# Performance work log

Measured on AMD Instinct MI355X. Metric: run time of the kernel, lower is better.

Reference implementation:

```python
import jax, jax.numpy as jnp
import numpy as np

N_NODES = 100000
N_EDGES = 3200000
N_FEATS = 512
HIDDEN = 16
N_CLASSES = 40


def gcn_conv(x, edge_index, W, b):
    """PyG-style GCNConv: linear -> symmetric-normalized scatter-add -> bias."""
    n = x.shape[0]
    src, dst = edge_index[0], edge_index[1]
    # add self-loops
    loop = jnp.arange(n, dtype=src.dtype)
    src = jnp.concatenate([src, loop])
    dst = jnp.concatenate([dst, loop])
    # symmetric normalization deg^{-1/2}[src] * deg^{-1/2}[dst]
    deg = jax.ops.segment_sum(jnp.ones_like(src, dtype=x.dtype), dst, num_segments=n)
    dinv = jnp.where(deg > 0, jax.lax.rsqrt(jnp.maximum(deg, 1.0)), 0.0)
    norm = dinv[src] * dinv[dst]  # [E+N]
    h = x @ W                     # [N, out]
    msg = h[src] * norm[:, None]  # gather + scale, [E+N, out]
    out = jax.ops.segment_sum(msg, dst, num_segments=n)  # scatter-add at targets
    return out + b


def setup_inputs() -> dict:
    key = jax.random.key(0)
    k1, k2, k3, k4 = jax.random.split(key, 4)
    x = jax.random.normal(k1, (N_NODES, N_FEATS), dtype=jnp.float32)
    edge_index = jax.random.randint(k2, (2, N_EDGES), 0, N_NODES, dtype=jnp.int64)
    # Glorot-ish scaled weights
    W1 = jax.random.normal(k3, (N_FEATS, HIDDEN), dtype=jnp.float32) * (1.0 / np.sqrt(N_FEATS))
    b1 = jnp.zeros((HIDDEN,), dtype=jnp.float32)
    W2 = jax.random.normal(k4, (HIDDEN, N_CLASSES), dtype=jnp.float32) * (1.0 / np.sqrt(HIDDEN))
    b2 = jnp.zeros((N_CLASSES,), dtype=jnp.float32)
    return {"x": x, "edge_index": edge_index, "W1": W1, "b1": b1, "W2": W2, "b2": b2}


def reference(x, edge_index, W1, b1, W2, b2):
    h = gcn_conv(x, edge_index, W1, b1)
    h = jax.nn.relu(h)
    # dropout is identity in eval mode
    h = gcn_conv(h, edge_index, W2, b2)
    return jax.nn.log_softmax(h, axis=1)
```

## Files before the change

kernel.cpp:

```cpp
#include <hip/hip_runtime.h>
#include <hip/hip_bf16.h>

#define NN 100000
#define NE 3200000
#define NF 512
#define NH 16
#define NC 40
#define NB 782
#define CAP 5120
#define NBLK 512
#define CHUNK 6250

typedef __attribute__((ext_vector_type(4))) float f32x4;
typedef __attribute__((ext_vector_type(8))) short bf16x8;

static __device__ __forceinline__ unsigned short f2b(float f) {
    unsigned int u = __float_as_uint(f);
    u += 0x7FFFu + ((u >> 16) & 1u);
    return (unsigned short)(u >> 16);
}
static __device__ __forceinline__ float b2f(unsigned short u) {
    return __uint_as_float(((unsigned int)u) << 16);
}


__global__ void __launch_bounds__(256) k_mshist(const int* __restrict__ ei,
                                                int* __restrict__ histG) {
    __shared__ int h[NB];
    for (int i = threadIdx.x; i < NB; i += 256) h[i] = 0;
    __syncthreads();
    int b = blockIdx.x;
    int e0 = b * CHUNK, e1 = min(NE, e0 + CHUNK);
    for (int e = e0 + threadIdx.x; e < e1; e += 256)
        atomicAdd(&h[((unsigned)ei[NE + e]) >> 7], 1);
    __syncthreads();
    for (int i = threadIdx.x; i < NB; i += 256)
        histG[b * NB + i] = h[i];
}


__global__ void __launch_bounds__(512) k_colscan(const int* __restrict__ histG,
                                                 int* __restrict__ ofsG,
                                                 int* __restrict__ bcnt) {
    __shared__ int sh[NBLK];
    int k = blockIdx.x;
    int t = threadIdx.x;
    int v = histG[t * NB + k];
    sh[t] = v;
    __syncthreads();
    for (int off = 1; off < NBLK; off <<= 1) {
        int add = (t >= off) ? sh[t - off] : 0;
        __syncthreads();
        sh[t] += add;
        __syncthreads();
    }
    ofsG[k * NBLK + t] = sh[t] - v;
    if (t == NBLK - 1) bcnt[k] = sh[t];
}


__global__ void k_bscan(const int* __restrict__ bcnt, int* __restrict__ bptr,
                        int* __restrict__ rowptr) {
    __shared__ int sh[1024];
    int t = threadIdx.x;
    int v = (t < NB) ? bcnt[t] : 0;
    sh[t] = v;
    __syncthreads();
    for (int off = 1; off < 1024; off <<= 1) {
        int add = (t >= off) ? sh[t - off] : 0;
        __syncthreads();
        sh[t] += add;
        __syncthreads();
    }
    if (t < NB) bptr[t] = sh[t] - v;
    if (t == 0) { bptr[NB] = NE; rowptr[NN] = NE; }
}


__global__ void __launch_bounds__(256) k_msscatter(const int* __restrict__ ei,
                                                   const int* __restrict__ bptr,
                                                   const int* __restrict__ ofsG,
                                                   unsigned int* __restrict__ pairs) {
    __shared__ int lcur[NB];
    int b = blockIdx.x;
    for (int k = threadIdx.x; k < NB; k += 256)
        lcur[k] = bptr[k] + ofsG[k * NBLK + b];
    __syncthreads();
    int e0 = b * CHUNK, e1 = min(NE, e0 + CHUNK);
    for (int e = e0 + threadIdx.x; e < e1; e += 256) {
        unsigned int s = (unsigned int)ei[e];
        unsigned int d = (unsigned int)ei[NE + e];
        int pos = atomicAdd(&lcur[d >> 7], 1);
        pairs[pos] = s | ((d & 127u) << 17);
    }
}


__global__ void __launch_bounds__(256) k_bsort(const unsigned int* __restrict__ pairs,
                                               const int* __restrict__ bptr,
                                               int* __restrict__ rowptr,
                                               float* __restrict__ dinv,
                                               int* __restrict__ ssrc) {
    __shared__ unsigned int ein[CAP];
    __shared__ unsigned int srt[CAP];
    __shared__ int lcnt[128], lofs[128], lcur[128];
    int b = blockIdx.x;
    int s0 = bptr[b], s1 = bptr[b + 1];
    int n = s1 - s0;
    for (int i = threadIdx.x; i < n; i += 256) ein[i] = pairs[s0 + i];
    if (threadIdx.x < 128) lcnt[threadIdx.x] = 0;
    __syncthreads();
    for (int i = threadIdx.x; i < n; i += 256) atomicAdd(&lcnt[ein[i] >> 17], 1);
    __syncthreads();
    if (threadIdx.x < 128) lofs[threadIdx.x] = lcnt[threadIdx.x];
    __syncthreads();
    for (int off = 1; off < 128; off <<= 1) {
        int add = 0;
        if (threadIdx.x < 128 && threadIdx.x >= off) add = lofs[threadIdx.x - off];
        __syncthreads();
        if (threadIdx.x < 128) lofs[threadIdx.x] += add;
        __syncthreads();
    }
    if (threadIdx.x < 128) {
        int excl = lofs[threadIdx.x] - lcnt[threadIdx.x];
        lcur[threadIdx.x] = excl;
        int node = b * 128 + threadIdx.x;
        if (node < NN) {
            rowptr[node] = s0 + excl;
            dinv[node] = rsqrtf((float)(lcnt[threadIdx.x] + 1));
        }
    }
    __syncthreads();
    for (int i = threadIdx.x; i < n; i += 256) {
        unsigned int v = ein[i];
        int pos = atomicAdd(&lcur[v >> 17], 1);
        srt[pos] = v & 0x1FFFFu;
    }
    __syncthreads();
    for (int i = threadIdx.x; i < n; i += 256) ssrc[s0 + i] = (int)srt[i];
}


__global__ void k_packW1(const float* __restrict__ W1, unsigned short* __restrict__ pack) {
    int idx = blockIdx.x * 256 + threadIdx.x;
    int s = idx >> 9;
    int l = (idx >> 3) & 63;
    int e = idx & 7;
    int k = s * 32 + (l >> 4) * 8 + e;
    int col = l & 15;
    pack[idx] = f2b(W1[k * 16 + col]);
}


__global__ void __launch_bounds__(256) k_gemm1(const float* __restrict__ x,
                                               const unsigned short* __restrict__ wp,
                                               const float* __restrict__ dinv,
                                               unsigned short* __restrict__ hs1) {
    int wave = threadIdx.x >> 6;
    int l = threadIdx.x & 63;
    int m0 = blockIdx.x * 64 + wave * 16;
    if (m0 >= NN) return;
    int row = m0 + (l & 15);
    int krow = (l >> 4) * 8;
    const float* xr = x + (size_t)row * NF + krow;
    const unsigned short* wl = wp + l * 8;

    f32x4 acc = {0.f, 0.f, 0.f, 0.f};
#pragma unroll 4
    for (int s = 0; s < 16; ++s) {
        f32x4 xa = *(const f32x4*)(xr + s * 32);
        f32x4 xb = *(const f32x4*)(xr + s * 32 + 4);
        union { bf16x8 v; unsigned short u[8]; } a;
        a.u[0] = f2b(xa.x); a.u[1] = f2b(xa.y); a.u[2] = f2b(xa.z); a.u[3] = f2b(xa.w);
        a.u[4] = f2b(xb.x); a.u[5] = f2b(xb.y); a.u[6] = f2b(xb.z); a.u[7] = f2b(xb.w);
        bf16x8 b = *(const bf16x8*)(wl + s * 512);
        acc = __builtin_amdgcn_mfma_f32_16x16x32_bf16(a.v, b, acc, 0, 0, 0);
    }
#pragma unroll
    for (int r = 0; r < 4; ++r) {
        int orow = m0 + (l >> 4) * 4 + r;
        hs1[(size_t)orow * NH + (l & 15)] = f2b(acc[r] * dinv[orow]);
    }
}


__global__ void __launch_bounds__(256) k_agg1(const unsigned short* __restrict__ hs,
                                              const int* __restrict__ rowptr,
                                              const int* __restrict__ ssrc,
                                              const float* __restrict__ dinv,
                                              const float* __restrict__ b1,
                                              unsigned short* __restrict__ r1) {
    int l = threadIdx.x & 63;
    int node = blockIdx.x * 4 + (threadIdx.x >> 6);
    int j = l & 15;
    int ec = l >> 4;
    float di = dinv[node];
    int s = rowptr[node];
    int e1 = rowptr[node + 1];
    float acc = (ec == 0) ? b2f(hs[(size_t)node * NH + j]) : 0.0f;
#pragma unroll 4
    for (int e = s + ec; e < e1; e += 4) {
        int src = ssrc[e];
        acc += b2f(hs[(size_t)src * NH + j]);
    }
    acc += __shfl_xor(acc, 16, 64);
    acc += __shfl_xor(acc, 32, 64);
    if (ec == 0) {
        float o = fmaxf(acc * di + b1[j], 0.0f) * di;
        r1[(size_t)node * NH + j] = f2b(o);
    }
}


__global__ void __launch_bounds__(256) k_agg2(const unsigned short* __restrict__ rs,
                                              const int* __restrict__ rowptr,
                                              const int* __restrict__ ssrc,
                                              const float* __restrict__ dinv,
                                              const float* __restrict__ W2,
                                              const float* __restrict__ b2,
                                              float* __restrict__ out) {
    __shared__ float w[NH * NC];
    __shared__ float bb[NC];
    int t = threadIdx.x;
    for (int i = t; i < NH * NC; i += 256) w[i] = W2[i];
    if (t < NC) bb[t] = b2[t];
    __syncthreads();
    int l = t & 63;
    int node = blockIdx.x * 4 + (t >> 6);
    int j = l & 15;
    int ec = l >> 4;
    float di = dinv[node];
    int s = rowptr[node];
    int e1 = rowptr[node + 1];
    float acc = (ec == 0) ? b2f(rs[(size_t)node * NH + j]) : 0.0f;
#pragma unroll 4
    for (int e = s + ec; e < e1; e += 4) {
        int src = ssrc[e];
        acc += b2f(rs[(size_t)src * NH + j]);
    }
    acc += __shfl_xor(acc, 16, 64);
    acc += __shfl_xor(acc, 32, 64);
    float zv = acc * di;
    float lg = (l < NC) ? bb[l] : -1e30f;
#pragma unroll
    for (int k = 0; k < NH; ++k) {
        float zk = __shfl(zv, k, 64);
        if (l < NC) lg += zk * w[k * NC + l];
    }
    float mx = lg;
#pragma unroll
    for (int off = 1; off < 64; off <<= 1) mx = fmaxf(mx, __shfl_xor(mx, off, 64));
    float ex = (l < NC) ? __expf(lg - mx) : 0.0f;
    float sm = ex;
#pragma unroll
    for (int off = 1; off < 64; off <<= 1) sm += __shfl_xor(sm, off, 64);
    if (l < NC) out[(size_t)node * NC + l] = lg - mx - __logf(sm);
}


extern "C" void kernel_launch(void* const* d_in, const int* in_sizes, int n_in,
                              void* d_out, int out_size, void* d_ws, size_t ws_size,
                              hipStream_t stream) {
    const float* x  = (const float*)d_in[0];
    const int*   ei = (const int*)d_in[1];
    const float* W1 = (const float*)d_in[2];
    const float* b1 = (const float*)d_in[3];
    const float* W2 = (const float*)d_in[4];
    const float* b2 = (const float*)d_in[5];
    float* out = (float*)d_out;

    char* ws = (char*)d_ws;
    size_t off = 0;
    auto alloc = [&](size_t bytes) -> void* {
        void* p = ws + off;
        off += (bytes + 255) & ~(size_t)255;
        return p;
    };
    int* histG      = (int*)alloc((size_t)NBLK * NB * 4);
    int* ofsG       = (int*)alloc((size_t)NB * NBLK * 4);
    int* bcnt       = (int*)alloc((size_t)NB * 4);
    int* bptr       = (int*)alloc((size_t)(NB + 1) * 4);
    int* rowptr     = (int*)alloc((size_t)(NN + 1) * 4);
    float* dinv     = (float*)alloc((size_t)NN * 4);
    unsigned short* w1p = (unsigned short*)alloc(16 * 64 * 8 * 2);
    unsigned int* pairs = (unsigned int*)alloc((size_t)NE * 4);
    int* ssrc       = (int*)alloc((size_t)NE * 4);
    unsigned short* h1  = (unsigned short*)alloc((size_t)NN * NH * 2);
    unsigned short* r1  = (unsigned short*)alloc((size_t)NN * NH * 2);

    k_packW1<<<32, 256, 0, stream>>>(W1, w1p);
    k_mshist<<<NBLK, 256, 0, stream>>>(ei, histG);
    k_colscan<<<NB, NBLK, 0, stream>>>(histG, ofsG, bcnt);
    k_bscan<<<1, 1024, 0, stream>>>(bcnt, bptr, rowptr);
    k_msscatter<<<NBLK, 256, 0, stream>>>(ei, bptr, ofsG, pairs);
    k_bsort<<<NB, 256, 0, stream>>>(pairs, bptr, rowptr, dinv, ssrc);
    k_gemm1<<<(NN + 63) / 64, 256, 0, stream>>>(x, w1p, dinv, h1);
    k_agg1<<<NN / 4, 256, 0, stream>>>(h1, rowptr, ssrc, dinv, b1, r1);
    k_agg2<<<NN / 4, 256, 0, stream>>>(r1, rowptr, ssrc, dinv, W2, b2, out);
}
```

Measured before the change: 248.5 us.

## Fuse GEMM1 with edge histogram in one launch and defer dinv scaling to aggregation

```diff
diff --git a/kernel.cpp b/kernel.cpp
--- a/kernel.cpp
+++ b/kernel.cpp
@@ -8,8 +8,9 @@
 #define NC 40
 #define NB 782
 #define CAP 5120
-#define NBLK 512
-#define CHUNK 6250
+#define NBLK 128
+#define CHUNK 25000
+#define GEMMB 1563
 
 typedef __attribute__((ext_vector_type(4))) float f32x4;
 typedef __attribute__((ext_vector_type(8))) short bf16x8;
@@ -24,38 +25,79 @@
 }
 
 
-__global__ void __launch_bounds__(256) k_mshist(const int* __restrict__ ei,
-                                                int* __restrict__ histG) {
-    __shared__ int h[NB];
-    for (int i = threadIdx.x; i < NB; i += 256) h[i] = 0;
-    __syncthreads();
-    int b = blockIdx.x;
-    int e0 = b * CHUNK, e1 = min(NE, e0 + CHUNK);
-    for (int e = e0 + threadIdx.x; e < e1; e += 256)
-        atomicAdd(&h[((unsigned)ei[NE + e]) >> 7], 1);
-    __syncthreads();
-    for (int i = threadIdx.x; i < NB; i += 256)
-        histG[b * NB + i] = h[i];
-}
-
-
-__global__ void __launch_bounds__(512) k_colscan(const int* __restrict__ histG,
+__global__ void __launch_bounds__(256) kA_gemm_hist(const float* __restrict__ x,
+                                                    const float* __restrict__ W1,
+                                                    const int* __restrict__ ei,
+                                                    unsigned short* __restrict__ h1,
+                                                    int* __restrict__ histG) {
+    __shared__ int smem[4096];
+    if (blockIdx.x < GEMMB) {
+        unsigned short* wl = (unsigned short*)smem;
+        for (int idx = threadIdx.x; idx < 8192; idx += 256) {
+            int s = idx >> 9;
+            int l = (idx >> 3) & 63;
+            int e = idx & 7;
+            int k = s * 32 + (l >> 4) * 8 + e;
+            wl[idx] = f2b(W1[k * 16 + (l & 15)]);
+        }
+        __syncthreads();
+        int wave = threadIdx.x >> 6;
+        int l = threadIdx.x & 63;
+        int m0 = blockIdx.x * 64 + wave * 16;
+        if (m0 >= NN) return;
+        int row = m0 + (l & 15);
+        int krow = (l >> 4) * 8;
+        const float* xr = x + (size_t)row * NF + krow;
+        const unsigned short* wf = wl + l * 8;
+        f32x4 acc = {0.f, 0.f, 0.f, 0.f};
+#pragma unroll 4
+        for (int s = 0; s < 16; ++s) {
+            f32x4 xa = *(const f32x4*)(xr + s * 32);
+            f32x4 xb = *(const f32x4*)(xr + s * 32 + 4);
+            union { bf16x8 v; unsigned short u[8]; } a;
+            a.u[0] = f2b(xa.x); a.u[1] = f2b(xa.y); a.u[2] = f2b(xa.z); a.u[3] = f2b(xa.w);
+            a.u[4] = f2b(xb.x); a.u[5] = f2b(xb.y); a.u[6] = f2b(xb.z); a.u[7] = f2b(xb.w);
+            bf16x8 b = *(const bf16x8*)(wf + s * 512);
+            acc = __builtin_amdgcn_mfma_f32_16x16x32_bf16(a.v, b, acc, 0, 0, 0);
+        }
+#pragma unroll
+        for (int r = 0; r < 4; ++r) {
+            int orow = m0 + (l >> 4) * 4 + r;
+            h1[(size_t)orow * NH + (l & 15)] = f2b(acc[r]);
+        }
+    } else {
+        int* h = smem;
+        for (int i = threadIdx.x; i < NB; i += 256) h[i] = 0;
+        __syncthreads();
+        int b = blockIdx.x - GEMMB;
+        int e0 = b * CHUNK, e1 = min(NE, e0 + CHUNK);
+        for (int e = e0 + threadIdx.x; e < e1; e += 256)
+            atomicAdd(&h[((unsigned)ei[NE + e]) >> 7], 1);
+        __syncthreads();
+        for (int i = threadIdx.x; i < NB; i += 256)
+            histG[b * NB + i] = h[i];
+    }
+}
+
+
+__global__ void __launch_bounds__(256) k_colscan(const int* __restrict__ histG,
                                                  int* __restrict__ ofsG,
                                                  int* __restrict__ bcnt) {
-    __shared__ int sh[NBLK];
-    int k = blockIdx.x;
+    __shared__ int sh[256];
     int t = threadIdx.x;
-    int v = histG[t * NB + k];
+    int k = blockIdx.x * 2 + (t >> 7);
+    int tt = t & 127;
+    int v = histG[tt * NB + k];
     sh[t] = v;
     __syncthreads();
-    for (int off = 1; off < NBLK; off <<= 1) {
-        int add = (t >= off) ? sh[t - off] : 0;
+    for (int off = 1; off < 128; off <<= 1) {
+        int add = (tt >= off) ? sh[t - off] : 0;
         __syncthreads();
         sh[t] += add;
         __syncthreads();
     }
-    ofsG[k * NBLK + t] = sh[t] - v;
-    if (t == NBLK - 1) bcnt[k] = sh[t];
+    ofsG[k * NBLK + tt] = sh[t] - v;
+    if (tt == 127) bcnt[k] = sh[t];
 }
 
 
@@ -77,17 +119,17 @@
 }
 
 
-__global__ void __launch_bounds__(256) k_msscatter(const int* __restrict__ ei,
-                                                   const int* __restrict__ bptr,
-                                                   const int* __restrict__ ofsG,
-                                                   unsigned int* __restrict__ pairs) {
+__global__ void __launch_bounds__(1024) k_msscatter(const int* __restrict__ ei,
+                                                    const int* __restrict__ bptr,
+                                                    const int* __restrict__ ofsG,
+                                                    unsigned int* __restrict__ pairs) {
     __shared__ int lcur[NB];
     int b = blockIdx.x;
-    for (int k = threadIdx.x; k < NB; k += 256)
+    for (int k = threadIdx.x; k < NB; k += 1024)
         lcur[k] = bptr[k] + ofsG[k * NBLK + b];
     __syncthreads();
     int e0 = b * CHUNK, e1 = min(NE, e0 + CHUNK);
-    for (int e = e0 + threadIdx.x; e < e1; e += 256) {
+    for (int e = e0 + threadIdx.x; e < e1; e += 1024) {
         unsigned int s = (unsigned int)ei[e];
         unsigned int d = (unsigned int)ei[NE + e];
         int pos = atomicAdd(&lcur[d >> 7], 1);
@@ -141,49 +183,6 @@
 }
 
 
-__global__ void k_packW1(const float* __restrict__ W1, unsigned short* __restrict__ pack) {
-    int idx = blockIdx.x * 256 + threadIdx.x;
-    int s = idx >> 9;
-    int l = (idx >> 3) & 63;
-    int e = idx & 7;
-    int k = s * 32 + (l >> 4) * 8 + e;
-    int col = l & 15;
-    pack[idx] = f2b(W1[k * 16 + col]);
-}
-
-
-__global__ void __launch_bounds__(256) k_gemm1(const float* __restrict__ x,
-                                               const unsigned short* __restrict__ wp,
-                                               const float* __restrict__ dinv,
-                                               unsigned short* __restrict__ hs1) {
-    int wave = threadIdx.x >> 6;
-    int l = threadIdx.x & 63;
-    int m0 = blockIdx.x * 64 + wave * 16;
-    if (m0 >= NN) return;
-    int row = m0 + (l & 15);
-    int krow = (l >> 4) * 8;
-    const float* xr = x + (size_t)row * NF + krow;
-    const unsigned short* wl = wp + l * 8;
-
-    f32x4 acc = {0.f, 0.f, 0.f, 0.f};
-#pragma unroll 4
-    for (int s = 0; s < 16; ++s) {
-        f32x4 xa = *(const f32x4*)(xr + s * 32);
-        f32x4 xb = *(const f32x4*)(xr + s * 32 + 4);
-        union { bf16x8 v; unsigned short u[8]; } a;
-        a.u[0] = f2b(xa.x); a.u[1] = f2b(xa.y); a.u[2] = f2b(xa.z); a.u[3] = f2b(xa.w);
-        a.u[4] = f2b(xb.x); a.u[5] = f2b(xb.y); a.u[6] = f2b(xb.z); a.u[7] = f2b(xb.w);
-        bf16x8 b = *(const bf16x8*)(wl + s * 512);
-        acc = __builtin_amdgcn_mfma_f32_16x16x32_bf16(a.v, b, acc, 0, 0, 0);
-    }
-#pragma unroll
-    for (int r = 0; r < 4; ++r) {
-        int orow = m0 + (l >> 4) * 4 + r;
-        hs1[(size_t)orow * NH + (l & 15)] = f2b(acc[r] * dinv[orow]);
-    }
-}
-
-
 __global__ void __launch_bounds__(256) k_agg1(const unsigned short* __restrict__ hs,
                                               const int* __restrict__ rowptr,
                                               const int* __restrict__ ssrc,
@@ -197,11 +196,11 @@
     float di = dinv[node];
     int s = rowptr[node];
     int e1 = rowptr[node + 1];
-    float acc = (ec == 0) ? b2f(hs[(size_t)node * NH + j]) : 0.0f;
+    float acc = (ec == 0) ? b2f(hs[(size_t)node * NH + j]) * di : 0.0f;
 #pragma unroll 4
     for (int e = s + ec; e < e1; e += 4) {
         int src = ssrc[e];
-        acc += b2f(hs[(size_t)src * NH + j]);
+        acc += b2f(hs[(size_t)src * NH + j]) * dinv[src];
     }
     acc += __shfl_xor(acc, 16, 64);
     acc += __shfl_xor(acc, 32, 64);
@@ -282,19 +281,16 @@
     int* bptr       = (int*)alloc((size_t)(NB + 1) * 4);
     int* rowptr     = (int*)alloc((size_t)(NN + 1) * 4);
     float* dinv     = (float*)alloc((size_t)NN * 4);
-    unsigned short* w1p = (unsigned short*)alloc(16 * 64 * 8 * 2);
     unsigned int* pairs = (unsigned int*)alloc((size_t)NE * 4);
     int* ssrc       = (int*)alloc((size_t)NE * 4);
     unsigned short* h1  = (unsigned short*)alloc((size_t)NN * NH * 2);
     unsigned short* r1  = (unsigned short*)alloc((size_t)NN * NH * 2);
 
-    k_packW1<<<32, 256, 0, stream>>>(W1, w1p);
-    k_mshist<<<NBLK, 256, 0, stream>>>(ei, histG);
-    k_colscan<<<NB, NBLK, 0, stream>>>(histG, ofsG, bcnt);
+    kA_gemm_hist<<<GEMMB + NBLK, 256, 0, stream>>>(x, W1, ei, h1, histG);
+    k_colscan<<<NB / 2, 256, 0, stream>>>(histG, ofsG, bcnt);
     k_bscan<<<1, 1024, 0, stream>>>(bcnt, bptr, rowptr);
-    k_msscatter<<<NBLK, 256, 0, stream>>>(ei, bptr, ofsG, pairs);
+    k_msscatter<<<NBLK, 1024, 0, stream>>>(ei, bptr, ofsG, pairs);
     k_bsort<<<NB, 256, 0, stream>>>(pairs, bptr, rowptr, dinv, ssrc);
-    k_gemm1<<<(NN + 63) / 64, 256, 0, stream>>>(x, w1p, dinv, h1);
     k_agg1<<<NN / 4, 256, 0, stream>>>(h1, rowptr, ssrc, dinv, b1, r1);
     k_agg2<<<NN / 4, 256, 0, stream>>>(r1, rowptr, ssrc, dinv, W2, b2, out);
 }
```

After: 257.9 us. 1.04x slower.
